# Optimization experiments

Hardware: AMD Instinct MI355X
Metric: run time of the kernel (lower is better)

The kernel has to match this reference:

```python
import jax, jax.numpy as jnp
import numpy as np

B, K, L, D, H, DFF, E = 4, 1024, 32, 128, 8, 512, 16384


def setup_inputs() -> dict:
    key = jax.random.key(0)
    ks = jax.random.split(key, 16)
    p = lambda k, sh: (jax.random.normal(k, sh, jnp.float32) * 0.02)
    return {
        "x": jax.random.normal(ks[0], (B, K, L, D), jnp.float32),
        "edge_index": jax.random.randint(ks[1], (B, 2, E), 0, K, jnp.int32),
        "edge_weight": jax.random.uniform(ks[2], (B, E), jnp.float32),
        "w_qkv": p(ks[3], (3 * D, D)), "b_qkv": p(ks[4], (3 * D,)),
        "w_out": p(ks[5], (D, D)), "b_out": p(ks[6], (D,)),
        "w1": p(ks[7], (DFF, D)), "b1": p(ks[8], (DFF,)),
        "w2": p(ks[9], (D, DFF)), "b2": p(ks[10], (D,)),
        "ln1_g": jnp.ones((D,), jnp.float32), "ln1_b": jnp.zeros((D,), jnp.float32),
        "ln2_g": jnp.ones((D,), jnp.float32), "ln2_b": jnp.zeros((D,), jnp.float32),
        "gcn_w": p(ks[11], (D, D)), "gcn_b": p(ks[12], (D,)),
    }


def _ln(x, g, b, eps=1e-5):
    m = x.mean(-1, keepdims=True)
    v = ((x - m) ** 2).mean(-1, keepdims=True)
    return (x - m) * jax.lax.rsqrt(v + eps) * g + b


def reference(x, edge_index, edge_weight, w_qkv, b_qkv, w_out, b_out,
              w1, b1, w2, b2, ln1_g, ln1_b, ln2_g, ln2_b, gcn_w, gcn_b):
    Bx, Kx, Lx, Dx = x.shape
    dh = Dx // H
    h = x.reshape(Bx * Kx, Lx, Dx)                       # [N, L, D], N = B*K
    # --- post-norm TransformerEncoderLayer (self-attn + FFN, relu, dropout=0) ---
    qkv = h @ w_qkv.T + b_qkv
    q, k_, v = jnp.split(qkv, 3, axis=-1)
    q = q.reshape(-1, Lx, H, dh)
    k_ = k_.reshape(-1, Lx, H, dh)
    v = v.reshape(-1, Lx, H, dh)
    scores = jnp.einsum('nlhd,nmhd->nhlm', q, k_) / np.float32(np.sqrt(dh))
    attn = jax.nn.softmax(scores, axis=-1)
    o = jnp.einsum('nhlm,nmhd->nlhd', attn, v).reshape(-1, Lx, Dx)
    o = o @ w_out.T + b_out
    h = _ln(h + o, ln1_g, ln1_b)
    ff = jax.nn.relu(h @ w1.T + b1) @ w2.T + b2
    h = _ln(h + ff, ln2_g, ln2_b)
    xt = h.reshape(Bx, Kx, Lx, Dx)
    # --- GCNConv (sym-normalized, self-loops) applied per (b, l) slice; batched over L ---
    self_idx = jnp.arange(Kx, dtype=edge_index.dtype)

    def gcn_one(xb, ei, ew):                              # xb [K, L, D]
        hh = xb @ gcn_w.T                                 # X W
        row = jnp.concatenate([ei[0], self_idx])          # sources (+ self loops)
        col = jnp.concatenate([ei[1], self_idx])          # targets
        w = jnp.concatenate([ew, jnp.ones((Kx,), ew.dtype)])
        deg = jax.ops.segment_sum(w, col, num_segments=Kx)
        deg_safe = jnp.where(deg > 0, deg, 1.0)
        dinv = jnp.where(deg > 0, jax.lax.rsqrt(deg_safe), 0.0)
        norm = dinv[row] * w * dinv[col]                  # [E+K]
        msg = hh[row] * norm[:, None, None]               # gather + scale
        return jax.ops.segment_sum(msg, col, num_segments=Kx) + gcn_b

    g = jax.vmap(gcn_one)(xt, edge_index, edge_weight)
    return xt + g
```

## Files before the change

### kernel.cpp

```cpp
#include <hip/hip_runtime.h>
#include <hip/hip_bf16.h>

#define BDIM 4
#define KDIM 1024
#define EDIM 16384
#define NSEQ (BDIM * KDIM)
#define REG  27136

typedef unsigned short ushort_t;
typedef unsigned int   uint32;

typedef __bf16 bf16x8 __attribute__((ext_vector_type(8)));
typedef float  f32x4  __attribute__((ext_vector_type(4)));

#define MFMA(A, B, C) __builtin_amdgcn_mfma_f32_16x16x32_bf16((A), (B), (C), 0, 0, 0)

__device__ __forceinline__ float bf2f(uint32 u) {
    union { uint32 i; float f; } v; v.i = u << 16; return v.f;
}
__device__ __forceinline__ ushort_t f2bf(float f) {
    union { float f; uint32 i; } v; v.f = f;
    uint32 r = (v.i + 0x7fffu + ((v.i >> 16) & 1u)) >> 16;
    return (ushort_t)r;
}
__device__ __forceinline__ uint32 cvtpk(float a, float b) {
    uint32 r;
    asm("v_cvt_pk_bf16_f32 %0, %1, %2" : "=v"(r) : "v"(a), "v"(b));
    return r;
}
__device__ __forceinline__ ushort_t f2bf_hw(float f) { return (ushort_t)cvtpk(f, f); }

__device__ __forceinline__ void unpack8(uint4 v, float* dst) {
    const uint32* pv = (const uint32*)&v;
#pragma unroll
    for (int q = 0; q < 4; q++) {
        uint32 w = pv[q];
        dst[2 * q]     = bf2f(w & 0xffffu);
        dst[2 * q + 1] = bf2f(w >> 16);
    }
}
__device__ __forceinline__ void store16bf(ushort_t* p, const float* v) {
    uint32 w[8];
#pragma unroll
    for (int q = 0; q < 8; q++) w[q] = cvtpk(v[2 * q], v[2 * q + 1]);
    ((uint4*)p)[0] = make_uint4(w[0], w[1], w[2], w[3]);
    ((uint4*)p)[1] = make_uint4(w[4], w[5], w[6], w[7]);
}

#define NWCVT 212992
__global__ void k_prep(const float* __restrict__ wq, const float* __restrict__ wo,
                       const float* __restrict__ w1, const float* __restrict__ w2,
                       const float* __restrict__ wg, ushort_t* __restrict__ dst) {
    int i = blockIdx.x * 256 + threadIdx.x;
    if (i >= NWCVT) return;
    float v;
    if      (i <  49152) v = wq[i];
    else if (i <  65536) v = wo[i - 49152];
    else if (i < 131072) v = w1[i - 65536];
    else if (i < 196608) v = w2[i - 131072];
    else                 v = wg[i - 196608];
    dst[i] = f2bf(v);
}

__global__ __launch_bounds__(256)
void k_transformer(const float* __restrict__ x,
                   const ushort_t* __restrict__ wq_bf, const float* __restrict__ b_qkv,
                   const ushort_t* __restrict__ wo_bf, const float* __restrict__ b_out,
                   const ushort_t* __restrict__ w1_bf, const float* __restrict__ b1,
                   const ushort_t* __restrict__ w2_bf, const float* __restrict__ b2,
                   const ushort_t* __restrict__ wg_bf,
                   const float* __restrict__ ln1g, const float* __restrict__ ln1b,
                   const float* __restrict__ ln2g, const float* __restrict__ ln2b,
                   float* __restrict__ out_xt, ushort_t* __restrict__ hh)
{
    const int n0   = blockIdx.x * 2;
    const int tid  = threadIdx.x;
    const int wave = tid >> 6;
    const int lane = tid & 63;
    const int lh   = lane & 15;
    const int lg   = lane >> 4;
    const int l    = tid >> 3;
    const int ds   = (tid & 7) * 16;

    __shared__ __align__(16) char smem[2 * REG];
#define SH(s)  ((ushort_t*)(smem + (s) * REG))
#define SVT(s) ((ushort_t*)(smem + (s) * REG))
#define SM(s)  ((ushort_t*)(smem + (s) * REG + 10240))
#define SMF(s) ((float*)(smem + (s) * REG + 10240))

#pragma unroll
    for (int s = 0; s < 2; s++) {
        const float4* px = (const float4*)(x + (size_t)(n0 + s) * 4096 + tid * 16);
        float h0[16];
#pragma unroll
        for (int q = 0; q < 4; q++) {
            float4 v = px[q];
            h0[4 * q] = v.x; h0[4 * q + 1] = v.y; h0[4 * q + 2] = v.z; h0[4 * q + 3] = v.w;
        }
        store16bf(SH(s) + l * 136 + ds, h0);
    }
    __syncthreads();

    {
        bf16x8 af[2][2][4];
#pragma unroll
        for (int s = 0; s < 2; s++)
#pragma unroll
            for (int mt = 0; mt < 2; mt++)
#pragma unroll
                for (int kk = 0; kk < 4; kk++)
                    af[s][mt][kk] = *(const bf16x8*)(SH(s) + (mt * 16 + lh) * 136 + kk * 32 + lg * 8);
        __syncthreads();

        const int ntb = wave * 6;
        float biasv[6];
#pragma unroll
        for (int j = 0; j < 6; j++) biasv[j] = b_qkv[(ntb + j) * 16 + lh];
#pragma unroll
        for (int j = 0; j < 6; j++) {
            bf16x8 bw[4];
#pragma unroll
            for (int kk = 0; kk < 4; kk++)
                bw[kk] = *(const bf16x8*)(wq_bf + (size_t)((ntb + j) * 16 + lh) * 128 + kk * 32 + lg * 8);
            f32x4 A[2][2];
#pragma unroll
            for (int s = 0; s < 2; s++) { A[s][0] = f32x4{0.f,0.f,0.f,0.f}; A[s][1] = f32x4{0.f,0.f,0.f,0.f}; }
#pragma unroll
            for (int kk = 0; kk < 4; kk++) {
#pragma unroll
                for (int s = 0; s < 2; s++) {
                    A[s][0] = MFMA(af[s][0][kk], bw[kk], A[s][0]);
                    A[s][1] = MFMA(af[s][1][kk], bw[kk], A[s][1]);
                }
            }
            const int nt  = ntb + j;
            const int col = nt * 16 + lh;
            const float bias = biasv[j];
#pragma unroll
            for (int s = 0; s < 2; s++) {
                if (nt < 16) {
                    const int r0 = lg * 4;
#pragma unroll
                    for (int i = 0; i < 4; i++) {
                        SM(s)[(r0 + i) * 264 + col]      = f2bf_hw(A[s][0][i] + bias);
                        SM(s)[(16 + r0 + i) * 264 + col] = f2bf_hw(A[s][1][i] + bias);
                    }
                } else {
                    const int vc = col - 256;
                    uint32 p01 = cvtpk(A[s][0][0] + bias, A[s][0][1] + bias);
                    uint32 p23 = cvtpk(A[s][0][2] + bias, A[s][0][3] + bias);
                    uint32 q01 = cvtpk(A[s][1][0] + bias, A[s][1][1] + bias);
                    uint32 q23 = cvtpk(A[s][1][2] + bias, A[s][1][3] + bias);
                    *(uint32*)&SVT(s)[vc * 40 + lg * 4]          = p01;
                    *(uint32*)&SVT(s)[vc * 40 + lg * 4 + 2]      = p23;
                    *(uint32*)&SVT(s)[vc * 40 + 16 + lg * 4]     = q01;
                    *(uint32*)&SVT(s)[vc * 40 + 16 + lg * 4 + 2] = q23;
                }
            }
        }
    }
    __syncthreads();

    {
        f32x4 sA[2][2][2][2];
        bf16x8 bz = {};
#pragma unroll
        for (int s = 0; s < 2; s++)
#pragma unroll
            for (int hd = 0; hd < 2; hd++) {
                const int h8 = wave * 2 + hd;
#pragma unroll
                for (int mt = 0; mt < 2; mt++) {
                    bf16x8 aq = *(const bf16x8*)(SM(s) + (mt * 16 + lh) * 264 + h8 * 16 + (lg & 1) * 8);
#pragma unroll
                    for (int nt = 0; nt < 2; nt++) {
                        bf16x8 bk = bz;
                        if (lg < 2)
                            bk = *(const bf16x8*)(SM(s) + (nt * 16 + lh) * 264 + 128 + h8 * 16 + lg * 8);
                        f32x4 z = {0.f,0.f,0.f,0.f};
                        sA[s][hd][mt][nt] = MFMA(aq, bk, z);
                    }
                }
            }
        __syncthreads();
#pragma unroll
        for (int s = 0; s < 2; s++)
#pragma unroll
            for (int hd = 0; hd < 2; hd++) {
                const int cb = hd ? (128 + wave * 32) : (wave * 32);
#pragma unroll
                for (int mt = 0; mt < 2; mt++) {
#pragma unroll
                    for (int i = 0; i < 4; i++) {
                        float e0 = __expf(sA[s][hd][mt][0][i] * 0.25f);
                        float e1 = __expf(sA[s][hd][mt][1][i] * 0.25f);
                        float sm = e0 + e1;
                        sm += __shfl_xor(sm, 1); sm += __shfl_xor(sm, 2);
                        sm += __shfl_xor(sm, 4); sm += __shfl_xor(sm, 8);
                        float inv = 1.0f / sm;
                        const int row = mt * 16 + lg * 4 + i;
                        SM(s)[row * 264 + cb + lh]      = f2bf_hw(e0 * inv);
                        SM(s)[row * 264 + cb + 16 + lh] = f2bf_hw(e1 * inv);
                    }
                }
            }
        __syncthreads();
        bf16x8 wbo[2][4];
#pragma unroll
        for (int j = 0; j < 2; j++)
#pragma unroll
            for (int kk = 0; kk < 4; kk++)
                wbo[j][kk] = *(const bf16x8*)(wo_bf + (size_t)((wave * 2 + j) * 16 + lh) * 128 + kk * 32 + lg * 8);
        float bo0 = b_out[(wave * 2 + 0) * 16 + lh];
        float bo1 = b_out[(wave * 2 + 1) * 16 + lh];
#pragma unroll
        for (int s = 0; s < 2; s++)
#pragma unroll
            for (int hd = 0; hd < 2; hd++) {
                const int h8 = wave * 2 + hd;
                const int cb = hd ? (128 + wave * 32) : (wave * 32);
                bf16x8 bv = *(const bf16x8*)(SVT(s) + (h8 * 16 + lh) * 40 + lg * 8);
#pragma unroll
                for (int mt = 0; mt < 2; mt++) {
                    bf16x8 ap = *(const bf16x8*)(SM(s) + (mt * 16 + lh) * 264 + cb + lg * 8);
                    f32x4 z = {0.f,0.f,0.f,0.f};
                    f32x4 o = MFMA(ap, bv, z);
                    const int r0 = mt * 16 + lg * 4, c = h8 * 16 + lh;
#pragma unroll
                    for (int i = 0; i < 4; i++)
                        SM(s)[(r0 + i) * 264 + c] = f2bf_hw(o[i]);
                }
            }
        __syncthreads();
#pragma unroll
        for (int s = 0; s < 2; s++) {
            bf16x8 af2[2][4];
#pragma unroll
            for (int mt = 0; mt < 2; mt++)
#pragma unroll
                for (int kk = 0; kk < 4; kk++)
                    af2[mt][kk] = *(const bf16x8*)(SM(s) + (mt * 16 + lh) * 264 + kk * 32 + lg * 8);
#pragma unroll
            for (int j = 0; j < 2; j++) {
                f32x4 a0 = {0.f,0.f,0.f,0.f}, a1 = {0.f,0.f,0.f,0.f};
#pragma unroll
                for (int kk = 0; kk < 4; kk++) {
                    a0 = MFMA(af2[0][kk], wbo[j][kk], a0);
                    a1 = MFMA(af2[1][kk], wbo[j][kk], a1);
                }
                const int col = (wave * 2 + j) * 16 + lh;
                const float bias = j ? bo1 : bo0;
#pragma unroll
                for (int i = 0; i < 4; i++) {
                    SH(s)[(lg * 4 + i) * 136 + col]      = f2bf_hw(a0[i] + bias);
                    SH(s)[(16 + lg * 4 + i) * 136 + col] = f2bf_hw(a1[i] + bias);
                }
            }
        }
        __syncthreads();
        {
            float g[16], be[16];
            {
                const float4* pg = (const float4*)(ln1g + ds);
                const float4* pb = (const float4*)(ln1b + ds);
#pragma unroll
                for (int q = 0; q < 4; q++) {
                    float4 vg = pg[q], vb = pb[q];
                    g[4*q]=vg.x; g[4*q+1]=vg.y; g[4*q+2]=vg.z; g[4*q+3]=vg.w;
                    be[4*q]=vb.x; be[4*q+1]=vb.y; be[4*q+2]=vb.z; be[4*q+3]=vb.w;
                }
            }
#pragma unroll
            for (int s = 0; s < 2; s++) {
                const float4* px = (const float4*)(x + (size_t)(n0 + s) * 4096 + tid * 16);
                float4 hx0 = px[0], hx1 = px[1], hx2 = px[2], hx3 = px[3];
                float h0v[16];
                { float4 v = hx0; h0v[0]=v.x; h0v[1]=v.y; h0v[2]=v.z; h0v[3]=v.w; }
                { float4 v = hx1; h0v[4]=v.x; h0v[5]=v.y; h0v[6]=v.z; h0v[7]=v.w; }
                { float4 v = hx2; h0v[8]=v.x; h0v[9]=v.y; h0v[10]=v.z; h0v[11]=v.w; }
                { float4 v = hx3; h0v[12]=v.x; h0v[13]=v.y; h0v[14]=v.z; h0v[15]=v.w; }
                float t[16]; float sum = 0.f;
#pragma unroll
                for (int i = 0; i < 16; i++) {
                    t[i] = h0v[i] + bf2f((uint32)SH(s)[l * 136 + ds + i]);
                    sum += t[i];
                }
                sum += __shfl_xor(sum, 1); sum += __shfl_xor(sum, 2); sum += __shfl_xor(sum, 4);
                float mean = sum * (1.f / 128.f);
                float vs = 0.f;
#pragma unroll
                for (int i = 0; i < 16; i++) { float d = t[i] - mean; vs += d * d; }
                vs += __shfl_xor(vs, 1); vs += __shfl_xor(vs, 2); vs += __shfl_xor(vs, 4);
                float rs = rsqrtf(vs * (1.f / 128.f) + 1e-5f);
                float h1v[16];
#pragma unroll
                for (int i = 0; i < 16; i++)
                    h1v[i] = (t[i] - mean) * rs * g[i] + be[i];
                store16bf(SH(s) + l * 136 + ds, h1v);
            }
        }
    }
    __syncthreads();

    f32x4 fa[2][4];
#pragma unroll
    for (int s = 0; s < 2; s++)
#pragma unroll
        for (int q = 0; q < 4; q++) fa[s][q] = f32x4{0.f,0.f,0.f,0.f};
    const int col0 = wave * 32 + lh, col1 = col0 + 16;
#pragma unroll
    for (int r = 0; r < 2; r++) {
#pragma unroll
        for (int s = 0; s < 2; s++) {
            bf16x8 ah[2][4];
#pragma unroll
            for (int mt = 0; mt < 2; mt++)
#pragma unroll
                for (int kk = 0; kk < 4; kk++)
                    ah[mt][kk] = *(const bf16x8*)(SH(s) + (mt * 16 + lh) * 136 + kk * 32 + lg * 8);
            float b1v[4];
#pragma unroll
            for (int j = 0; j < 4; j++) b1v[j] = b1[(r * 16 + wave * 4 + j) * 16 + lh];
#pragma unroll
            for (int j = 0; j < 4; j++) {
                bf16x8 bw[4];
                {
                    const int nt = (r * 16 + wave * 4 + j) * 16 + lh;
#pragma unroll
                    for (int kk = 0; kk < 4; kk++)
                        bw[kk] = *(const bf16x8*)(w1_bf + (size_t)nt * 128 + kk * 32 + lg * 8);
                }
                f32x4 a0 = {0.f,0.f,0.f,0.f}, a1 = {0.f,0.f,0.f,0.f};
#pragma unroll
                for (int kk = 0; kk < 4; kk++) {
                    a0 = MFMA(ah[0][kk], bw[kk], a0);
                    a1 = MFMA(ah[1][kk], bw[kk], a1);
                }
                const float bias = b1v[j];
                const int cl = (wave * 4 + j) * 16 + lh;
                const int r0 = lg * 4;
#pragma unroll
                for (int i = 0; i < 4; i++) {
                    SM(s)[(r0 + i) * 264 + cl]      = f2bf_hw(fmaxf(a0[i] + bias, 0.f));
                    SM(s)[(16 + r0 + i) * 264 + cl] = f2bf_hw(fmaxf(a1[i] + bias, 0.f));
                }
            }
        }
        __syncthreads();
#pragma unroll
        for (int kk = 0; kk < 8; kk++) {
            bf16x8 wp0 = *(const bf16x8*)(w2_bf + (size_t)col0 * 512 + r * 256 + kk * 32 + lg * 8);
            bf16x8 wp1 = *(const bf16x8*)(w2_bf + (size_t)col1 * 512 + r * 256 + kk * 32 + lg * 8);
#pragma unroll
            for (int s = 0; s < 2; s++) {
                bf16x8 a0 = *(const bf16x8*)(SM(s) + lh * 264 + kk * 32 + lg * 8);
                bf16x8 a1 = *(const bf16x8*)(SM(s) + (16 + lh) * 264 + kk * 32 + lg * 8);
                fa[s][0] = MFMA(a0, wp0, fa[s][0]);
                fa[s][1] = MFMA(a1, wp0, fa[s][1]);
                fa[s][2] = MFMA(a0, wp1, fa[s][2]);
                fa[s][3] = MFMA(a1, wp1, fa[s][3]);
            }
        }
        __syncthreads();
    }
    {
        const float bi0 = b2[col0], bi1 = b2[col1];
#pragma unroll
        for (int s = 0; s < 2; s++) {
#pragma unroll
            for (int i = 0; i < 4; i++) {
                SMF(s)[(lg * 4 + i) * 132 + col0]      = fa[s][0][i] + bi0;
                SMF(s)[(16 + lg * 4 + i) * 132 + col0] = fa[s][1][i] + bi0;
                SMF(s)[(lg * 4 + i) * 132 + col1]      = fa[s][2][i] + bi1;
                SMF(s)[(16 + lg * 4 + i) * 132 + col1] = fa[s][3][i] + bi1;
            }
        }
    }
    __syncthreads();

    {
        float g[16], be[16];
        {
            const float4* pg = (const float4*)(ln2g + ds);
            const float4* pb = (const float4*)(ln2b + ds);
#pragma unroll
            for (int q = 0; q < 4; q++) {
                float4 vg = pg[q], vb = pb[q];
                g[4*q]=vg.x; g[4*q+1]=vg.y; g[4*q+2]=vg.z; g[4*q+3]=vg.w;
                be[4*q]=vb.x; be[4*q+1]=vb.y; be[4*q+2]=vb.z; be[4*q+3]=vb.w;
            }
        }
#pragma unroll
        for (int s = 0; s < 2; s++) {
            float t[16]; float sum = 0.f;
#pragma unroll
            for (int i = 0; i < 16; i++) {
                t[i] = bf2f((uint32)SH(s)[l * 136 + ds + i]) + SMF(s)[l * 132 + ds + i];
                sum += t[i];
            }
            sum += __shfl_xor(sum, 1); sum += __shfl_xor(sum, 2); sum += __shfl_xor(sum, 4);
            float mean = sum * (1.f / 128.f);
            float vs = 0.f;
#pragma unroll
            for (int i = 0; i < 16; i++) { float d = t[i] - mean; vs += d * d; }
            vs += __shfl_xor(vs, 1); vs += __shfl_xor(vs, 2); vs += __shfl_xor(vs, 4);
            float rs = rsqrtf(vs * (1.f / 128.f) + 1e-5f);
            float h2v[16];
#pragma unroll
            for (int i = 0; i < 16; i++)
                h2v[i] = (t[i] - mean) * rs * g[i] + be[i];
            float4* po = (float4*)(out_xt + (size_t)(n0 + s) * 4096 + tid * 16);
#pragma unroll
            for (int q = 0; q < 4; q++)
                po[q] = make_float4(h2v[4 * q], h2v[4 * q + 1], h2v[4 * q + 2], h2v[4 * q + 3]);
            store16bf(SH(s) + l * 136 + ds, h2v);
        }
    }
    __syncthreads();

    {
        bf16x8 wb[2][4];
#pragma unroll
        for (int j = 0; j < 2; j++)
#pragma unroll
            for (int kk = 0; kk < 4; kk++)
                wb[j][kk] = *(const bf16x8*)(wg_bf + (size_t)((wave * 2 + j) * 16 + lh) * 128 + kk * 32 + lg * 8);
#pragma unroll
        for (int s = 0; s < 2; s++) {
            bf16x8 ag[2][4];
#pragma unroll
            for (int mt = 0; mt < 2; mt++)
#pragma unroll
                for (int kk = 0; kk < 4; kk++)
                    ag[mt][kk] = *(const bf16x8*)(SH(s) + (mt * 16 + lh) * 136 + kk * 32 + lg * 8);
            ushort_t* hp = hh + (size_t)(n0 + s) * 4096;
#pragma unroll
            for (int j = 0; j < 2; j++) {
                f32x4 a0 = {0.f,0.f,0.f,0.f}, a1 = {0.f,0.f,0.f,0.f};
#pragma unroll
                for (int kk = 0; kk < 4; kk++) {
                    a0 = MFMA(ag[0][kk], wb[j][kk], a0);
                    a1 = MFMA(ag[1][kk], wb[j][kk], a1);
                }
                const int col = (wave * 2 + j) * 16 + lh;
                const int r0 = lg * 4;
#pragma unroll
                for (int i = 0; i < 4; i++) {
                    hp[(r0 + i) * 128 + col]      = f2bf_hw(a0[i]);
                    hp[(16 + r0 + i) * 128 + col] = f2bf_hw(a1[i]);
                }
            }
        }
    }
#undef SH
#undef SVT
#undef SM
#undef SMF
}

__global__ void k_init(float* deg, int* count) {
    int i = blockIdx.x * 256 + threadIdx.x;
    if (i < BDIM * KDIM) { deg[i] = 1.0f; count[i] = 0; }
}

__global__ void k_degcount(const int* __restrict__ ei, const float* __restrict__ ew,
                           float* deg, int* count) {
    int idx = blockIdx.x * 256 + threadIdx.x;
    if (idx >= BDIM * EDIM) return;
    int b = idx / EDIM, e = idx - b * EDIM;
    int col = ei[(size_t)b * 2 * EDIM + EDIM + e];
    float w = ew[(size_t)b * EDIM + e];
    atomicAdd(&deg[b * KDIM + col], w);
    atomicAdd(&count[b * KDIM + col], 1);
}

__global__ __launch_bounds__(1024)
void k_scan(const int* __restrict__ count, int* offs, int* cursor) {
    __shared__ int s[KDIM];
    int b = blockIdx.x, i = threadIdx.x;
    int c = count[b * KDIM + i];
    s[i] = c; __syncthreads();
#pragma unroll 1
    for (int off = 1; off < KDIM; off <<= 1) {
        int t = (i >= off) ? s[i - off] : 0;
        __syncthreads();
        s[i] += t;
        __syncthreads();
    }
    int excl = s[i] - c;
    offs[b * KDIM + i] = excl;
    cursor[b * KDIM + i] = excl;
}

__global__ void k_fill(const int* __restrict__ ei, int* cursor, int* elist) {
    int idx = blockIdx.x * 256 + threadIdx.x;
    if (idx >= BDIM * EDIM) return;
    int b = idx / EDIM, e = idx - b * EDIM;
    int col = ei[(size_t)b * 2 * EDIM + EDIM + e];
    int pos = atomicAdd(&cursor[b * KDIM + col], 1);
    elist[(size_t)b * EDIM + pos] = e;
}

__global__ __launch_bounds__(256)
void k_gather(const int* __restrict__ ei, const float* __restrict__ ew,
              const float* __restrict__ deg, const int* __restrict__ offs,
              const int* __restrict__ count, const int* __restrict__ elist,
              const ushort_t* __restrict__ hh, const float* __restrict__ gcn_b,
              float* __restrict__ out)
{
    const int node = blockIdx.x;
    const int b = node >> 10, i = node & 1023;
    const int tid = threadIdx.x;
    const float dcol = rsqrtf(deg[node]);
    const int off = offs[node], cnt = count[node];
    const ushort_t* hhb = hh + ((size_t)b * KDIM) * 4096;
    const int* elb = elist + (size_t)b * EDIM;
    const int* eib = ei + (size_t)b * 2 * EDIM;
    const float* ewb = ew + (size_t)b * EDIM;
    const float* degb = deg + b * KDIM;

    float acc[16];
    {
        const uint4* ph = (const uint4*)(hhb + (size_t)i * 4096 + tid * 16);
        uint4 a = ph[0], bb = ph[1];
        float tmp[16]; unpack8(a, tmp); unpack8(bb, tmp + 8);
        float nrm = dcol * dcol;
#pragma unroll
        for (int k = 0; k < 16; k++) acc[k] = tmp[k] * nrm;
    }
    if (cnt > 0) {
        int e_cur = elb[off];
        int row_cur = eib[e_cur];
        float w_cur = ewb[e_cur];
        for (int t = 0; t < cnt; t++) {
            int e_nxt = 0, row_nxt = 0; float w_nxt = 0.f;
            if (t + 1 < cnt) {
                e_nxt = elb[off + t + 1];
                row_nxt = eib[e_nxt];
                w_nxt = ewb[e_nxt];
            }
            float nrm = rsqrtf(degb[row_cur]) * w_cur * dcol;
            const uint4* ph = (const uint4*)(hhb + (size_t)row_cur * 4096 + tid * 16);
            uint4 a = ph[0], bb = ph[1];
            float tmp[16]; unpack8(a, tmp); unpack8(bb, tmp + 8);
#pragma unroll
            for (int k = 0; k < 16; k++) acc[k] += tmp[k] * nrm;
            e_cur = e_nxt; row_cur = row_nxt; w_cur = w_nxt;
        }
    }
    const int d0 = (tid * 16) & 127;
    float4* po = (float4*)(out + (size_t)node * 4096 + tid * 16);
#pragma unroll
    for (int q = 0; q < 4; q++) {
        float4 xo = po[q];
        xo.x += acc[4 * q]     + gcn_b[d0 + 4 * q];
        xo.y += acc[4 * q + 1] + gcn_b[d0 + 4 * q + 1];
        xo.z += acc[4 * q + 2] + gcn_b[d0 + 4 * q + 2];
        xo.w += acc[4 * q + 3] + gcn_b[d0 + 4 * q + 3];
        po[q] = xo;
    }
}

extern "C" void kernel_launch(void* const* d_in, const int* in_sizes, int n_in,
                              void* d_out, int out_size, void* d_ws, size_t ws_size,
                              hipStream_t stream) {
    const float* x     = (const float*)d_in[0];
    const int*   ei    = (const int*)d_in[1];
    const float* ew    = (const float*)d_in[2];
    const float* w_qkv = (const float*)d_in[3];
    const float* b_qkv = (const float*)d_in[4];
    const float* w_out = (const float*)d_in[5];
    const float* b_out = (const float*)d_in[6];
    const float* w1    = (const float*)d_in[7];
    const float* b1    = (const float*)d_in[8];
    const float* w2    = (const float*)d_in[9];
    const float* b2    = (const float*)d_in[10];
    const float* ln1g  = (const float*)d_in[11];
    const float* ln1b  = (const float*)d_in[12];
    const float* ln2g  = (const float*)d_in[13];
    const float* ln2b  = (const float*)d_in[14];
    const float* gcnw  = (const float*)d_in[15];
    const float* gcnb  = (const float*)d_in[16];
    float* out = (float*)d_out;

    char* ws = (char*)d_ws;
    ushort_t* wbf   = (ushort_t*)ws;
    ushort_t* wq_bf = wbf;
    ushort_t* wo_bf = wbf + 49152;
    ushort_t* w1_bf = wbf + 65536;
    ushort_t* w2_bf = wbf + 131072;
    ushort_t* wg_bf = wbf + 196608;
    float*    deg   = (float*)(ws + 425984);
    int*      count = (int*)(ws + 442368);
    int*      offs  = (int*)(ws + 458752);
    int*      cursor= (int*)(ws + 475136);
    int*      elist = (int*)(ws + 491520);
    ushort_t* hh    = (ushort_t*)(ws + 753664);

    k_prep<<<(NWCVT + 255) / 256, 256, 0, stream>>>(w_qkv, w_out, w1, w2, gcnw, wbf);
    k_init<<<16, 256, 0, stream>>>(deg, count);
    k_transformer<<<NSEQ / 2, 256, 0, stream>>>(x, wq_bf, b_qkv, wo_bf, b_out,
                                                w1_bf, b1, w2_bf, b2, wg_bf,
                                                ln1g, ln1b, ln2g, ln2b, out, hh);
    k_degcount<<<256, 256, 0, stream>>>(ei, ew, deg, count);
    k_scan<<<BDIM, 1024, 0, stream>>>(count, offs, cursor);
    k_fill<<<256, 256, 0, stream>>>(ei, cursor, elist);
    k_gather<<<NSEQ, 256, 0, stream>>>(ei, ew, deg, offs, count, elist, hh, gcnb, out);
}
```

Before: 306.9 us.

## Shrink LDS row padding and software-prefetch neighbor rows in GCN gather

Reduces shared-memory row strides in the fused transformer kernel (264→260, 40→36, 132→130) and moves the M region offset, shrinking per-block LDS so more blocks may fit per CU. In the GCN aggregation kernel, the loop now prefetches the next neighbor's feature row one iteration ahead and the edge index two ahead, overlapping dependent global loads with accumulation. The new strides may change LDS bank-conflict patterns, and the prefetch raises register pressure.

```diff
diff --git a/kernel.cpp b/kernel.cpp
--- a/kernel.cpp
+++ b/kernel.cpp
@@ -5,7 +5,8 @@
 #define KDIM 1024
 #define EDIM 16384
 #define NSEQ (BDIM * KDIM)
-#define REG  27136
+#define REG  25856
+#define MOFF 9216
 
 typedef unsigned short ushort_t;
 typedef unsigned int   uint32;
@@ -85,8 +86,8 @@
     __shared__ __align__(16) char smem[2 * REG];
 #define SH(s)  ((ushort_t*)(smem + (s) * REG))
 #define SVT(s) ((ushort_t*)(smem + (s) * REG))
-#define SM(s)  ((ushort_t*)(smem + (s) * REG + 10240))
-#define SMF(s) ((float*)(smem + (s) * REG + 10240))
+#define SM(s)  ((ushort_t*)(smem + (s) * REG + MOFF))
+#define SMF(s) ((float*)(smem + (s) * REG + MOFF))
 
 #pragma unroll
     for (int s = 0; s < 2; s++) {
@@ -142,8 +143,8 @@
                     const int r0 = lg * 4;
 #pragma unroll
                     for (int i = 0; i < 4; i++) {
-                        SM(s)[(r0 + i) * 264 + col]      = f2bf_hw(A[s][0][i] + bias);
-                        SM(s)[(16 + r0 + i) * 264 + col] = f2bf_hw(A[s][1][i] + bias);
+                        SM(s)[(r0 + i) * 260 + col]      = f2bf_hw(A[s][0][i] + bias);
+                        SM(s)[(16 + r0 + i) * 260 + col] = f2bf_hw(A[s][1][i] + bias);
                     }
                 } else {
                     const int vc = col - 256;
@@ -151,10 +152,10 @@
                     uint32 p23 = cvtpk(A[s][0][2] + bias, A[s][0][3] + bias);
                     uint32 q01 = cvtpk(A[s][1][0] + bias, A[s][1][1] + bias);
                     uint32 q23 = cvtpk(A[s][1][2] + bias, A[s][1][3] + bias);
-                    *(uint32*)&SVT(s)[vc * 40 + lg * 4]          = p01;
-                    *(uint32*)&SVT(s)[vc * 40 + lg * 4 + 2]      = p23;
-                    *(uint32*)&SVT(s)[vc * 40 + 16 + lg * 4]     = q01;
-                    *(uint32*)&SVT(s)[vc * 40 + 16 + lg * 4 + 2] = q23;
+                    *(uint32*)&SVT(s)[vc * 36 + lg * 4]          = p01;
+                    *(uint32*)&SVT(s)[vc * 36 + lg * 4 + 2]      = p23;
+                    *(uint32*)&SVT(s)[vc * 36 + 16 + lg * 4]     = q01;
+                    *(uint32*)&SVT(s)[vc * 36 + 16 + lg * 4 + 2] = q23;
                 }
             }
         }
@@ -171,12 +172,12 @@
                 const int h8 = wave * 2 + hd;
 #pragma unroll
                 for (int mt = 0; mt < 2; mt++) {
-                    bf16x8 aq = *(const bf16x8*)(SM(s) + (mt * 16 + lh) * 264 + h8 * 16 + (lg & 1) * 8);
+                    bf16x8 aq = *(const bf16x8*)(SM(s) + (mt * 16 + lh) * 260 + h8 * 16 + (lg & 1) * 8);
 #pragma unroll
                     for (int nt = 0; nt < 2; nt++) {
                         bf16x8 bk = bz;
                         if (lg < 2)
-                            bk = *(const bf16x8*)(SM(s) + (nt * 16 + lh) * 264 + 128 + h8 * 16 + lg * 8);
+                            bk = *(const bf16x8*)(SM(s) + (nt * 16 + lh) * 260 + 128 + h8 * 16 + lg * 8);
                         f32x4 z = {0.f,0.f,0.f,0.f};
                         sA[s][hd][mt][nt] = MFMA(aq, bk, z);
                     }
@@ -199,8 +200,8 @@
                         sm += __shfl_xor(sm, 4); sm += __shfl_xor(sm, 8);
                         float inv = 1.0f / sm;
                         const int row = mt * 16 + lg * 4 + i;
-                        SM(s)[row * 264 + cb + lh]      = f2bf_hw(e0 * inv);
-                        SM(s)[row * 264 + cb + 16 + lh] = f2bf_hw(e1 * inv);
+                        SM(s)[row * 260 + cb + lh]      = f2bf_hw(e0 * inv);
+                        SM(s)[row * 260 + cb + 16 + lh] = f2bf_hw(e1 * inv);
                     }
                 }
             }
@@ -219,16 +220,16 @@
             for (int hd = 0; hd < 2; hd++) {
                 const int h8 = wave * 2 + hd;
                 const int cb = hd ? (128 + wave * 32) : (wave * 32);
-                bf16x8 bv = *(const bf16x8*)(SVT(s) + (h8 * 16 + lh) * 40 + lg * 8);
+                bf16x8 bv = *(const bf16x8*)(SVT(s) + (h8 * 16 + lh) * 36 + lg * 8);
 #pragma unroll
                 for (int mt = 0; mt < 2; mt++) {
-                    bf16x8 ap = *(const bf16x8*)(SM(s) + (mt * 16 + lh) * 264 + cb + lg * 8);
+                    bf16x8 ap = *(const bf16x8*)(SM(s) + (mt * 16 + lh) * 260 + cb + lg * 8);
                     f32x4 z = {0.f,0.f,0.f,0.f};
                     f32x4 o = MFMA(ap, bv, z);
                     const int r0 = mt * 16 + lg * 4, c = h8 * 16 + lh;
 #pragma unroll
                     for (int i = 0; i < 4; i++)
-                        SM(s)[(r0 + i) * 264 + c] = f2bf_hw(o[i]);
+                        SM(s)[(r0 + i) * 260 + c] = f2bf_hw(o[i]);
                 }
             }
         __syncthreads();
@@ -239,7 +240,7 @@
             for (int mt = 0; mt < 2; mt++)
 #pragma unroll
                 for (int kk = 0; kk < 4; kk++)
-                    af2[mt][kk] = *(const bf16x8*)(SM(s) + (mt * 16 + lh) * 264 + kk * 32 + lg * 8);
+                    af2[mt][kk] = *(const bf16x8*)(SM(s) + (mt * 16 + lh) * 260 + kk * 32 + lg * 8);
 #pragma unroll
             for (int j = 0; j < 2; j++) {
                 f32x4 a0 = {0.f,0.f,0.f,0.f}, a1 = {0.f,0.f,0.f,0.f};
@@ -341,8 +342,8 @@
                 const int r0 = lg * 4;
 #pragma unroll
                 for (int i = 0; i < 4; i++) {
-                    SM(s)[(r0 + i) * 264 + cl]      = f2bf_hw(fmaxf(a0[i] + bias, 0.f));
-                    SM(s)[(16 + r0 + i) * 264 + cl] = f2bf_hw(fmaxf(a1[i] + bias, 0.f));
+                    SM(s)[(r0 + i) * 260 + cl]      = f2bf_hw(fmaxf(a0[i] + bias, 0.f));
+                    SM(s)[(16 + r0 + i) * 260 + cl] = f2bf_hw(fmaxf(a1[i] + bias, 0.f));
                 }
             }
         }
@@ -353,8 +354,8 @@
             bf16x8 wp1 = *(const bf16x8*)(w2_bf + (size_t)col1 * 512 + r * 256 + kk * 32 + lg * 8);
 #pragma unroll
             for (int s = 0; s < 2; s++) {
-                bf16x8 a0 = *(const bf16x8*)(SM(s) + lh * 264 + kk * 32 + lg * 8);
-                bf16x8 a1 = *(const bf16x8*)(SM(s) + (16 + lh) * 264 + kk * 32 + lg * 8);
+                bf16x8 a0 = *(const bf16x8*)(SM(s) + lh * 260 + kk * 32 + lg * 8);
+                bf16x8 a1 = *(const bf16x8*)(SM(s) + (16 + lh) * 260 + kk * 32 + lg * 8);
                 fa[s][0] = MFMA(a0, wp0, fa[s][0]);
                 fa[s][1] = MFMA(a1, wp0, fa[s][1]);
                 fa[s][2] = MFMA(a0, wp1, fa[s][2]);
@@ -369,10 +370,10 @@
         for (int s = 0; s < 2; s++) {
 #pragma unroll
             for (int i = 0; i < 4; i++) {
-                SMF(s)[(lg * 4 + i) * 132 + col0]      = fa[s][0][i] + bi0;
-                SMF(s)[(16 + lg * 4 + i) * 132 + col0] = fa[s][1][i] + bi0;
-                SMF(s)[(lg * 4 + i) * 132 + col1]      = fa[s][2][i] + bi1;
-                SMF(s)[(16 + lg * 4 + i) * 132 + col1] = fa[s][3][i] + bi1;
+                SMF(s)[(lg * 4 + i) * 130 + col0]      = fa[s][0][i] + bi0;
+                SMF(s)[(16 + lg * 4 + i) * 130 + col0] = fa[s][1][i] + bi0;
+                SMF(s)[(lg * 4 + i) * 130 + col1]      = fa[s][2][i] + bi1;
+                SMF(s)[(16 + lg * 4 + i) * 130 + col1] = fa[s][3][i] + bi1;
             }
         }
     }
@@ -395,7 +396,7 @@
             float t[16]; float sum = 0.f;
 #pragma unroll
             for (int i = 0; i < 16; i++) {
-                t[i] = bf2f((uint32)SH(s)[l * 136 + ds + i]) + SMF(s)[l * 132 + ds + i];
+                t[i] = bf2f((uint32)SH(s)[l * 136 + ds + i]) + SMF(s)[l * 130 + ds + i];
                 sum += t[i];
             }
             sum += __shfl_xor(sum, 1); sum += __shfl_xor(sum, 2); sum += __shfl_xor(sum, 4);
@@ -529,23 +530,36 @@
         for (int k = 0; k < 16; k++) acc[k] = tmp[k] * nrm;
     }
     if (cnt > 0) {
-        int e_cur = elb[off];
-        int row_cur = eib[e_cur];
-        float w_cur = ewb[e_cur];
+        int e0 = elb[off];
+        int row_cur = eib[e0];
+        float w_cur = ewb[e0];
+        const uint4* ph0 = (const uint4*)(hhb + (size_t)row_cur * 4096 + tid * 16);
+        uint4 a_cur = ph0[0], b_cur = ph0[1];
+        int row_nxt = 0; float w_nxt = 0.f;
+        if (cnt > 1) {
+            int e1 = elb[off + 1];
+            row_nxt = eib[e1];
+            w_nxt = ewb[e1];
+        }
         for (int t = 0; t < cnt; t++) {
-            int e_nxt = 0, row_nxt = 0; float w_nxt = 0.f;
+            uint4 a_nxt = make_uint4(0,0,0,0), b_nxt = make_uint4(0,0,0,0);
             if (t + 1 < cnt) {
-                e_nxt = elb[off + t + 1];
-                row_nxt = eib[e_nxt];
-                w_nxt = ewb[e_nxt];
+                const uint4* ph1 = (const uint4*)(hhb + (size_t)row_nxt * 4096 + tid * 16);
+                a_nxt = ph1[0]; b_nxt = ph1[1];
+            }
+            int row_n2 = 0; float w_n2 = 0.f;
+            if (t + 2 < cnt) {
+                int e2 = elb[off + t + 2];
+                row_n2 = eib[e2];
+                w_n2 = ewb[e2];
             }
             float nrm = rsqrtf(degb[row_cur]) * w_cur * dcol;
-            const uint4* ph = (const uint4*)(hhb + (size_t)row_cur * 4096 + tid * 16);
-            uint4 a = ph[0], bb = ph[1];
-            float tmp[16]; unpack8(a, tmp); unpack8(bb, tmp + 8);
+            float tmp[16]; unpack8(a_cur, tmp); unpack8(b_cur, tmp + 8);
 #pragma unroll
             for (int k = 0; k < 16; k++) acc[k] += tmp[k] * nrm;
-            e_cur = e_nxt; row_cur = row_nxt; w_cur = w_nxt;
+            a_cur = a_nxt; b_cur = b_nxt;
+            row_cur = row_nxt; w_cur = w_nxt;
+            row_nxt = row_n2; w_nxt = w_n2;
         }
     }
     const int d0 = (tid * 16) & 127;
```

Result: faster. 299.7 us (-2.3%).
